# Optimization experiments

Hardware: AMD Instinct MI355X
Metric: run time of the kernel (lower is better)

## Reference

```python
import jax, jax.numpy as jnp
import numpy as np
from jax import lax

WINDOW = 8
MAX_VAL = 1.0
C1 = (0.01 * MAX_VAL) ** 2
C2 = (0.03 * MAX_VAL) ** 2


def _box_sum(x):
    # Equivalent to conv2d with an all-ones WINDOW x WINDOW kernel, groups=C, VALID padding.
    return lax.reduce_window(x, 0.0, lax.add,
                             window_dimensions=(1, 1, WINDOW, WINDOW),
                             window_strides=(1, 1, 1, 1),
                             padding='VALID')


def setup_inputs() -> dict:
    key = jax.random.key(0)
    k1, k2 = jax.random.split(key)
    shape = (32, 3, 512, 512)  # NCHW, C=3 per groups=3 conv
    groundtruth = jax.random.uniform(k1, shape, dtype=jnp.float32)
    noisy_img = jax.random.uniform(k2, shape, dtype=jnp.float32)
    return {"groundtruth": groundtruth, "noisy_img": noisy_img}


def reference(groundtruth, noisy_img):
    mu1 = _box_sum(groundtruth)
    mu2 = _box_sum(noisy_img)
    mu1_sq = mu1 * mu1
    mu2_sq = mu2 * mu2
    mu1_mu2 = mu1 * mu2
    sigma1_sq = _box_sum(groundtruth * groundtruth) - mu1_sq
    sigma2_sq = _box_sum(noisy_img * noisy_img) - mu2_sq
    sigma12 = _box_sum(groundtruth * noisy_img) - mu1_mu2
    ssim_map = ((2.0 * mu1_mu2 + C1) * (2.0 * sigma12 + C2)) / (
        (mu1_sq + mu2_sq + C1) * (sigma1_sq + sigma2_sq + C2))
    return jnp.mean(1.0 - ssim_map)
```

## Files before the change

### kernel.cpp

```cpp
#include <hip/hip_runtime.h>


#define W 512
#define H 512
#define OW 505
#define OH 505
#define TH 16
#define NSTRIP ((OH + TH - 1) / TH)
#define NIMG 96
#define NPIX (96.0 * 505.0 * 505.0)

__device__ __forceinline__ float4 ld4(const float* p) { return *(const float4*)p; }
__device__ __forceinline__ float4 f4add(float4 a, float4 b) {
    return make_float4(a.x + b.x, a.y + b.y, a.z + b.z, a.w + b.w);
}
__device__ __forceinline__ float4 f4sub(float4 a, float4 b) {
    return make_float4(a.x - b.x, a.y - b.y, a.z - b.z, a.w - b.w);
}
__device__ __forceinline__ float4 f4mul(float4 a, float4 b) {
    return make_float4(a.x * b.x, a.y * b.y, a.z * b.z, a.w * b.w);
}

__global__ void finalize(const double* p, float* out) {
    out[0] = 1.0f - (float)(*p / NPIX);
}

__global__ void __launch_bounds__(128, 2)
ssim_main(const float* __restrict__ gt, const float* __restrict__ ni,
          double* __restrict__ acc_out)
{
    const int t   = threadIdx.x;
    const int c0  = t * 4;
    const int img = blockIdx.y;
    const int R0  = blockIdx.x * TH;
    const int R1  = min(R0 + TH, OH);

    const float C1 = 1e-4f;
    const float C2 = 9e-4f;

    const float* gx = gt + (size_t)img * (W * H) + c0;
    const float* gy = ni + (size_t)img * (W * H) + c0;

    __shared__ float vbuf[4][4][520];
    __shared__ float wpart[2];

    float4 ring_x[8], ring_y[8];
    float4 vsx = make_float4(0, 0, 0, 0);
    float4 vsy = make_float4(0, 0, 0, 0);
    float4 vsq = make_float4(0, 0, 0, 0);
    float4 vsp = make_float4(0, 0, 0, 0);

#pragma unroll
    for (int k = 0; k < 7; ++k) {
        float4 x = ld4(gx + (size_t)(R0 + k) * W);
        float4 y = ld4(gy + (size_t)(R0 + k) * W);
        ring_x[k] = x; ring_y[k] = y;
        vsx = f4add(vsx, x);
        vsy = f4add(vsy, y);
        vsq = f4add(vsq, f4add(f4mul(x, x), f4mul(y, y)));
        vsp = f4add(vsp, f4mul(x, y));
    }
    ring_x[7] = make_float4(0, 0, 0, 0);
    ring_y[7] = make_float4(0, 0, 0, 0);

    float4 pfx[4], pfy[4];
#pragma unroll
    for (int m = 0; m < 4; ++m) {
        pfx[m] = ld4(gx + (size_t)(R0 + 7 + m) * W);
        pfy[m] = ld4(gy + (size_t)(R0 + 7 + m) * W);
    }

    float acc = 0.0f;

#define PHASEA_ROW(rb, m, slot) {                                         \
        if ((rb) + (m) < R1) {                         \
            float4 cx = pfx[m], cy = pfy[m];                              \
            float4 ox = ring_x[slot], oy = ring_y[slot];                  \
            vsx = f4add(f4sub(vsx, ox), cx);                              \
            vsy = f4add(f4sub(vsy, oy), cy);                              \
            vsq = f4add(vsq, f4sub(f4add(f4mul(cx, cx), f4mul(cy, cy)),   \
                                   f4add(f4mul(ox, ox), f4mul(oy, oy)))); \
            vsp = f4add(vsp, f4sub(f4mul(cx, cy), f4mul(ox, oy)));        \
            ring_x[slot] = cx; ring_y[slot] = cy;                         \
            *(float4*)&vbuf[m][0][c0] = vsx;                              \
            *(float4*)&vbuf[m][1][c0] = vsy;                              \
            *(float4*)&vbuf[m][2][c0] = vsq;                              \
            *(float4*)&vbuf[m][3][c0] = vsp;                              \
        }                                                                 \
    }

#define HORIZ(q) {                                                        \
        float4 o = *(float4*)&vbuf[m][q][c0];                             \
        float4 a = *(float4*)&vbuf[m][q][c0 + 4];                         \
        float4 e = *(float4*)&vbuf[m][q][c0 + 8];                         \
        float s = ((o.x + o.y) + (o.z + o.w)) +                           \
                  ((a.x + a.y) + (a.z + a.w));                            \
        B[q][0] = s;                                                      \
        s += e.x - o.x; B[q][1] = s;                                      \
        s += e.y - o.y; B[q][2] = s;                                      \
        s += e.z - o.z; B[q][3] = s;                                      \
    }

#define PHASEB_ROW(rb, mm) {                                              \
        if ((rb) + (mm) < R1) {                        \
            const int m = (mm);                                           \
            float B[4][4];                                                \
            HORIZ(0) HORIZ(1) HORIZ(2) HORIZ(3)                           \
            _Pragma("unroll")                                             \
            for (int j = 0; j < 4; ++j) {                                 \
                float Sx = B[0][j], Sy = B[1][j];                         \
                float Sq = B[2][j], Sp = B[3][j];                         \
                float mu12 = Sx * Sy;                                     \
                float n1v = 2.0f * mu12 + C1;                             \
                float n2v = 2.0f * (Sp - mu12) + C2;                      \
                float sx2 = Sx * Sx, sy2 = Sy * Sy;                       \
                float d1  = sx2 + sy2 + C1;                               \
                float d2  = (Sq - sx2 - sy2) + C2;                        \
                float sv  = (n1v * n2v) * __builtin_amdgcn_rcpf(d1 * d2); \
                if (c0 + j < OW) acc += sv;                               \
            }                                                             \
        }                                                                 \
    }

#define GROUP(rb, s0, s1, s2, s3) {                                       \
        if ((rb) < R1) {                               \
            PHASEA_ROW(rb, 0, s0) PHASEA_ROW(rb, 1, s1)                   \
            PHASEA_ROW(rb, 2, s2) PHASEA_ROW(rb, 3, s3)                   \
            __syncthreads();                                              \
            _Pragma("unroll")                                             \
            for (int m = 0; m < 4; ++m) {      \
                if ((rb) + 4 + m < R1) {                                  \
                    pfx[m] = ld4(gx + (size_t)((rb) + 11 + m) * W);       \
                    pfy[m] = ld4(gy + (size_t)((rb) + 11 + m) * W);       \
                }                                                         \
            }                                                             \
            PHASEB_ROW(rb, 0) PHASEB_ROW(rb, 1)                           \
            PHASEB_ROW(rb, 2) PHASEB_ROW(rb, 3)                           \
            __syncthreads();                                              \
        }                                                                 \
    }

    for (int rb0 = R0; rb0 < R1; rb0 += 8) {
        GROUP(rb0,     7, 0, 1, 2)
        GROUP(rb0 + 4, 3, 4, 5, 6)
    }

#pragma unroll
    for (int off = 32; off > 0; off >>= 1) acc += __shfl_down(acc, off);
    const int wave = t >> 6, lane = t & 63;
    if (lane == 0) wpart[wave] = acc;
    __syncthreads();
    if (t == 0) atomicAdd(acc_out, (double)(wpart[0] + wpart[1]));
}

extern "C" void kernel_launch(void* const* d_in, const int* in_sizes, int n_in,
                              void* d_out, int out_size, void* d_ws, size_t ws_size,
                              hipStream_t stream) {
    const float* gt = (const float*)d_in[0];
    const float* ni = (const float*)d_in[1];
    double* acc = (double*)d_ws;

    hipMemsetAsync(acc, 0, sizeof(double), stream);
    dim3 grid(NSTRIP, NIMG);
    ssim_main<<<grid, 128, 0, stream>>>(gt, ni, acc);
    finalize<<<1, 1, 0, stream>>>(acc, (float*)d_out);
}
```

Before: 232.8 us.

## Process two rows per group with lighter barriers and higher occupancy

Each group now handles two output rows instead of four, which halves the shared vertical-sum buffer and the prefetch registers. Launch bounds are raised to allow four blocks per CU. __syncthreads is replaced by a barrier that waits only on LDS counters, so outstanding global prefetch loads are not drained at each barrier. The cost is twice as many barriers per row, and prefetch now runs only two rows ahead, which shortens the latency-hiding window.

```diff
diff --git a/kernel.cpp b/kernel.cpp
--- a/kernel.cpp
+++ b/kernel.cpp
@@ -21,11 +21,16 @@
     return make_float4(a.x * b.x, a.y * b.y, a.z * b.z, a.w * b.w);
 }
 
+__device__ __forceinline__ void wbar() {
+    asm volatile("s_waitcnt lgkmcnt(0)" ::: "memory");
+    __builtin_amdgcn_s_barrier();
+}
+
 __global__ void finalize(const double* p, float* out) {
     out[0] = 1.0f - (float)(*p / NPIX);
 }
 
-__global__ void __launch_bounds__(128, 2)
+__global__ void __launch_bounds__(128, 4)
 ssim_main(const float* __restrict__ gt, const float* __restrict__ ni,
           double* __restrict__ acc_out)
 {
@@ -41,7 +46,7 @@
     const float* gx = gt + (size_t)img * (W * H) + c0;
     const float* gy = ni + (size_t)img * (W * H) + c0;
 
-    __shared__ float vbuf[4][4][520];
+    __shared__ float vbuf[2][4][520];
     __shared__ float wpart[2];
 
     float4 ring_x[8], ring_y[8];
@@ -63,12 +68,11 @@
     ring_x[7] = make_float4(0, 0, 0, 0);
     ring_y[7] = make_float4(0, 0, 0, 0);
 
-    float4 pfx[4], pfy[4];
-#pragma unroll
-    for (int m = 0; m < 4; ++m) {
-        pfx[m] = ld4(gx + (size_t)(R0 + 7 + m) * W);
-        pfy[m] = ld4(gy + (size_t)(R0 + 7 + m) * W);
-    }
+    float4 pfx[2], pfy[2];
+    pfx[0] = ld4(gx + (size_t)(R0 + 7) * W);
+    pfy[0] = ld4(gy + (size_t)(R0 + 7) * W);
+    pfx[1] = ld4(gx + (size_t)(R0 + 8) * W);
+    pfy[1] = ld4(gy + (size_t)(R0 + 8) * W);
 
     float acc = 0.0f;
 
@@ -122,27 +126,28 @@
         }                                                                 \
     }
 
-#define GROUP(rb, s0, s1, s2, s3) {                                       \
+#define GROUP2(rb, s0, s1) {                                              \
         if ((rb) < R1) {                               \
             PHASEA_ROW(rb, 0, s0) PHASEA_ROW(rb, 1, s1)                   \
-            PHASEA_ROW(rb, 2, s2) PHASEA_ROW(rb, 3, s3)                   \
-            __syncthreads();                                              \
-            _Pragma("unroll")                                             \
-            for (int m = 0; m < 4; ++m) {      \
-                if ((rb) + 4 + m < R1) {                                  \
-                    pfx[m] = ld4(gx + (size_t)((rb) + 11 + m) * W);       \
-                    pfy[m] = ld4(gy + (size_t)((rb) + 11 + m) * W);       \
-                }                                                         \
+            wbar();                                                       \
+            if ((rb) + 2 < R1) {                                          \
+                pfx[0] = ld4(gx + (size_t)((rb) + 9) * W);                \
+                pfy[0] = ld4(gy + (size_t)((rb) + 9) * W);                \
+            }                                                             \
+            if ((rb) + 3 < R1) {                                          \
+                pfx[1] = ld4(gx + (size_t)((rb) + 10) * W);               \
+                pfy[1] = ld4(gy + (size_t)((rb) + 10) * W);               \
             }                                                             \
             PHASEB_ROW(rb, 0) PHASEB_ROW(rb, 1)                           \
-            PHASEB_ROW(rb, 2) PHASEB_ROW(rb, 3)                           \
-            __syncthreads();                                              \
+            wbar();                                                       \
         }                                                                 \
     }
 
     for (int rb0 = R0; rb0 < R1; rb0 += 8) {
-        GROUP(rb0,     7, 0, 1, 2)
-        GROUP(rb0 + 4, 3, 4, 5, 6)
+        GROUP2(rb0,     7, 0)
+        GROUP2(rb0 + 2, 1, 2)
+        GROUP2(rb0 + 4, 3, 4)
+        GROUP2(rb0 + 6, 5, 6)
     }
 
 #pragma unroll
```

After: 251.1 us. 1.08x slower.

## Replace shared-memory horizontal sums with wave shuffles, single-wave blocks

Applied to the files above, without the earlier changes.

Each block becomes a single 64-lane wave where every lane owns 8 columns, so a row of 512 fits in one wave. The horizontal window sum now reads the neighbour lane's vertical sums through shuffles instead of shared memory, which removes the LDS buffer and both __syncthreads per row group. The ring buffer of old rows is dropped: the row leaving the window is reloaded from global memory (expected to hit cache). Costs are twice the loads per row and higher register pressure from holding 8 columns of 4 sums per lane.

```diff
diff --git a/kernel.cpp b/kernel.cpp
--- a/kernel.cpp
+++ b/kernel.cpp
@@ -11,26 +11,22 @@
 #define NPIX (96.0 * 505.0 * 505.0)
 
 __device__ __forceinline__ float4 ld4(const float* p) { return *(const float4*)p; }
-__device__ __forceinline__ float4 f4add(float4 a, float4 b) {
-    return make_float4(a.x + b.x, a.y + b.y, a.z + b.z, a.w + b.w);
-}
-__device__ __forceinline__ float4 f4sub(float4 a, float4 b) {
-    return make_float4(a.x - b.x, a.y - b.y, a.z - b.z, a.w - b.w);
-}
-__device__ __forceinline__ float4 f4mul(float4 a, float4 b) {
-    return make_float4(a.x * b.x, a.y * b.y, a.z * b.z, a.w * b.w);
-}
 
 __global__ void finalize(const double* p, float* out) {
     out[0] = 1.0f - (float)(*p / NPIX);
 }
 
-__global__ void __launch_bounds__(128, 2)
+#define UNPACK8(a0, a1, dst) {                                            \
+        dst[0] = a0.x; dst[1] = a0.y; dst[2] = a0.z; dst[3] = a0.w;       \
+        dst[4] = a1.x; dst[5] = a1.y; dst[6] = a1.z; dst[7] = a1.w;       \
+    }
+
+__global__ void __launch_bounds__(64, 4)
 ssim_main(const float* __restrict__ gt, const float* __restrict__ ni,
           double* __restrict__ acc_out)
 {
-    const int t   = threadIdx.x;
-    const int c0  = t * 4;
+    const int l   = threadIdx.x;
+    const int c0  = l * 8;
     const int img = blockIdx.y;
     const int R0  = blockIdx.x * TH;
     const int R1  = min(R0 + TH, OH);
@@ -41,116 +37,133 @@
     const float* gx = gt + (size_t)img * (W * H) + c0;
     const float* gy = ni + (size_t)img * (W * H) + c0;
 
-    __shared__ float vbuf[4][4][520];
-    __shared__ float wpart[2];
+    float vsx[8], vsy[8], vsq[8], vsp[8];
+#pragma unroll
+    for (int j = 0; j < 8; ++j) { vsx[j] = 0.f; vsy[j] = 0.f; vsq[j] = 0.f; vsp[j] = 0.f; }
 
-    float4 ring_x[8], ring_y[8];
-    float4 vsx = make_float4(0, 0, 0, 0);
-    float4 vsy = make_float4(0, 0, 0, 0);
-    float4 vsq = make_float4(0, 0, 0, 0);
-    float4 vsp = make_float4(0, 0, 0, 0);
+    float4 pix0, pix1, piy0, piy1;
+    float4 pox0, pox1, poy0, poy1;
 
-#pragma unroll
-    for (int k = 0; k < 7; ++k) {
-        float4 x = ld4(gx + (size_t)(R0 + k) * W);
-        float4 y = ld4(gy + (size_t)(R0 + k) * W);
-        ring_x[k] = x; ring_y[k] = y;
-        vsx = f4add(vsx, x);
-        vsy = f4add(vsy, y);
-        vsq = f4add(vsq, f4add(f4mul(x, x), f4mul(y, y)));
-        vsp = f4add(vsp, f4mul(x, y));
-    }
-    ring_x[7] = make_float4(0, 0, 0, 0);
-    ring_y[7] = make_float4(0, 0, 0, 0);
-
-    float4 pfx[4], pfy[4];
-#pragma unroll
-    for (int m = 0; m < 4; ++m) {
-        pfx[m] = ld4(gx + (size_t)(R0 + 7 + m) * W);
-        pfy[m] = ld4(gy + (size_t)(R0 + 7 + m) * W);
+    {
+        const float* px = gx + (size_t)R0 * W;
+        const float* py = gy + (size_t)R0 * W;
+        pix0 = ld4(px); pix1 = ld4(px + 4);
+        piy0 = ld4(py); piy1 = ld4(py + 4);
     }
 
     float acc = 0.0f;
 
-#define PHASEA_ROW(rb, m, slot) {                                         \
-        if ((rb) + (m) < R1) {                         \
-            float4 cx = pfx[m], cy = pfy[m];                              \
-            float4 ox = ring_x[slot], oy = ring_y[slot];                  \
-            vsx = f4add(f4sub(vsx, ox), cx);                              \
-            vsy = f4add(f4sub(vsy, oy), cy);                              \
-            vsq = f4add(vsq, f4sub(f4add(f4mul(cx, cx), f4mul(cy, cy)),   \
-                                   f4add(f4mul(ox, ox), f4mul(oy, oy)))); \
-            vsp = f4add(vsp, f4sub(f4mul(cx, cy), f4mul(ox, oy)));        \
-            ring_x[slot] = cx; ring_y[slot] = cy;                         \
-            *(float4*)&vbuf[m][0][c0] = vsx;                              \
-            *(float4*)&vbuf[m][1][c0] = vsy;                              \
-            *(float4*)&vbuf[m][2][c0] = vsq;                              \
-            *(float4*)&vbuf[m][3][c0] = vsp;                              \
+#pragma unroll 1
+    for (int r = R0; r < R0 + 7; ++r) {
+        float cx[8], cy[8];
+        UNPACK8(pix0, pix1, cx)
+        UNPACK8(piy0, piy1, cy)
+        {
+            const float* px = gx + (size_t)(r + 1) * W;
+            const float* py = gy + (size_t)(r + 1) * W;
+            pix0 = ld4(px); pix1 = ld4(px + 4);
+            piy0 = ld4(py); piy1 = ld4(py + 4);
+        }
+#pragma unroll
+        for (int j = 0; j < 8; ++j) {
+            vsx[j] = vsx[j] + cx[j];
+            vsy[j] = vsy[j] + cy[j];
+            vsq[j] = vsq[j] + (cx[j] * cx[j] + cy[j] * cy[j]);
+            vsp[j] = vsp[j] + cx[j] * cy[j];
+        }
+    }
+
+#define HORIZ_SSIM() {                                                    \
+        float nx[8], ny[8], nq[8], np_[8];                                \
+        _Pragma("unroll")                                                 \
+        for (int j = 0; j < 8; ++j) {                                     \
+            nx[j]  = __shfl_down(vsx[j], 1);                              \
+            ny[j]  = __shfl_down(vsy[j], 1);                              \
+            nq[j]  = __shfl_down(vsq[j], 1);                              \
+            np_[j] = __shfl_down(vsp[j], 1);                              \
+        }                                                                 \
+        float Sx = ((vsx[0] + vsx[1]) + (vsx[2] + vsx[3])) +              \
+                   ((vsx[4] + vsx[5]) + (vsx[6] + vsx[7]));               \
+        float Sy = ((vsy[0] + vsy[1]) + (vsy[2] + vsy[3])) +              \
+                   ((vsy[4] + vsy[5]) + (vsy[6] + vsy[7]));               \
+        float Sq = ((vsq[0] + vsq[1]) + (vsq[2] + vsq[3])) +              \
+                   ((vsq[4] + vsq[5]) + (vsq[6] + vsq[7]));               \
+        float Sp = ((vsp[0] + vsp[1]) + (vsp[2] + vsp[3])) +              \
+                   ((vsp[4] + vsp[5]) + (vsp[6] + vsp[7]));               \
+        _Pragma("unroll")                                                 \
+        for (int j = 0; j < 8; ++j) {                                     \
+            if (j) {                                                      \
+                Sx += nx[j-1] - vsx[j-1];                                 \
+                Sy += ny[j-1] - vsy[j-1];                                 \
+                Sq += nq[j-1] - vsq[j-1];                                 \
+                Sp += np_[j-1] - vsp[j-1];                                \
+            }                                                             \
+            float mu12 = Sx * Sy;                                         \
+            float n1v = 2.0f * mu12 + C1;                                 \
+            float n2v = 2.0f * (Sp - mu12) + C2;                          \
+            float sx2 = Sx * Sx, sy2 = Sy * Sy;                           \
+            float d1  = sx2 + sy2 + C1;                                   \
+            float d2  = (Sq - sx2 - sy2) + C2;                            \
+            float sv  = (n1v * n2v) * __builtin_amdgcn_rcpf(d1 * d2);     \
+            if (c0 + j < OW) acc += sv;                                   \
         }                                                                 \
     }
 
-#define HORIZ(q) {                                                        \
-        float4 o = *(float4*)&vbuf[m][q][c0];                             \
-        float4 a = *(float4*)&vbuf[m][q][c0 + 4];                         \
-        float4 e = *(float4*)&vbuf[m][q][c0 + 8];                         \
-        float s = ((o.x + o.y) + (o.z + o.w)) +                           \
-                  ((a.x + a.y) + (a.z + a.w));                            \
-        B[q][0] = s;                                                      \
-        s += e.x - o.x; B[q][1] = s;                                      \
-        s += e.y - o.y; B[q][2] = s;                                      \
-        s += e.z - o.z; B[q][3] = s;                                      \
+    {
+        float cx[8], cy[8];
+        UNPACK8(pix0, pix1, cx)
+        UNPACK8(piy0, piy1, cy)
+        {
+            const float* px = gx + (size_t)(R0 + 8) * W;
+            const float* py = gy + (size_t)(R0 + 8) * W;
+            pix0 = ld4(px); pix1 = ld4(px + 4);
+            piy0 = ld4(py); piy1 = ld4(py + 4);
+            const float* qx = gx + (size_t)R0 * W;
+            const float* qy = gy + (size_t)R0 * W;
+            pox0 = ld4(qx); pox1 = ld4(qx + 4);
+            poy0 = ld4(qy); poy1 = ld4(qy + 4);
+        }
+#pragma unroll
+        for (int j = 0; j < 8; ++j) {
+            vsx[j] = vsx[j] + cx[j];
+            vsy[j] = vsy[j] + cy[j];
+            vsq[j] = vsq[j] + (cx[j] * cx[j] + cy[j] * cy[j]);
+            vsp[j] = vsp[j] + cx[j] * cy[j];
+        }
+        HORIZ_SSIM()
     }
 
-#define PHASEB_ROW(rb, mm) {                                              \
-        if ((rb) + (mm) < R1) {                        \
-            const int m = (mm);                                           \
-            float B[4][4];                                                \
-            HORIZ(0) HORIZ(1) HORIZ(2) HORIZ(3)                           \
-            _Pragma("unroll")                                             \
-            for (int j = 0; j < 4; ++j) {                                 \
-                float Sx = B[0][j], Sy = B[1][j];                         \
-                float Sq = B[2][j], Sp = B[3][j];                         \
-                float mu12 = Sx * Sy;                                     \
-                float n1v = 2.0f * mu12 + C1;                             \
-                float n2v = 2.0f * (Sp - mu12) + C2;                      \
-                float sx2 = Sx * Sx, sy2 = Sy * Sy;                       \
-                float d1  = sx2 + sy2 + C1;                               \
-                float d2  = (Sq - sx2 - sy2) + C2;                        \
-                float sv  = (n1v * n2v) * __builtin_amdgcn_rcpf(d1 * d2); \
-                if (c0 + j < OW) acc += sv;                               \
-            }                                                             \
-        }                                                                 \
-    }
-
-#define GROUP(rb, s0, s1, s2, s3) {                                       \
-        if ((rb) < R1) {                               \
-            PHASEA_ROW(rb, 0, s0) PHASEA_ROW(rb, 1, s1)                   \
-            PHASEA_ROW(rb, 2, s2) PHASEA_ROW(rb, 3, s3)                   \
-            __syncthreads();                                              \
-            _Pragma("unroll")                                             \
-            for (int m = 0; m < 4; ++m) {      \
-                if ((rb) + 4 + m < R1) {                                  \
-                    pfx[m] = ld4(gx + (size_t)((rb) + 11 + m) * W);       \
-                    pfy[m] = ld4(gy + (size_t)((rb) + 11 + m) * W);       \
-                }                                                         \
-            }                                                             \
-            PHASEB_ROW(rb, 0) PHASEB_ROW(rb, 1)                           \
-            PHASEB_ROW(rb, 2) PHASEB_ROW(rb, 3)                           \
-            __syncthreads();                                              \
-        }                                                                 \
-    }
-
-    for (int rb0 = R0; rb0 < R1; rb0 += 8) {
-        GROUP(rb0,     7, 0, 1, 2)
-        GROUP(rb0 + 4, 3, 4, 5, 6)
+#pragma unroll 1
+    for (int o = R0 + 1; o < R1; ++o) {
+        float cx[8], cy[8], ox[8], oy[8];
+        UNPACK8(pix0, pix1, cx)
+        UNPACK8(piy0, piy1, cy)
+        UNPACK8(pox0, pox1, ox)
+        UNPACK8(poy0, poy1, oy)
+        if (o + 1 < R1) {
+            const float* px = gx + (size_t)(o + 8) * W;
+            const float* py = gy + (size_t)(o + 8) * W;
+            pix0 = ld4(px); pix1 = ld4(px + 4);
+            piy0 = ld4(py); piy1 = ld4(py + 4);
+            const float* qx = gx + (size_t)o * W;
+            const float* qy = gy + (size_t)o * W;
+            pox0 = ld4(qx); pox1 = ld4(qx + 4);
+            poy0 = ld4(qy); poy1 = ld4(qy + 4);
+        }
+#pragma unroll
+        for (int j = 0; j < 8; ++j) {
+            vsx[j] = (vsx[j] - ox[j]) + cx[j];
+            vsy[j] = (vsy[j] - oy[j]) + cy[j];
+            vsq[j] = vsq[j] + ((cx[j] * cx[j] + cy[j] * cy[j]) -
+                               (ox[j] * ox[j] + oy[j] * oy[j]));
+            vsp[j] = vsp[j] + (cx[j] * cy[j] - ox[j] * oy[j]);
+        }
+        HORIZ_SSIM()
     }
 
 #pragma unroll
     for (int off = 32; off > 0; off >>= 1) acc += __shfl_down(acc, off);
-    const int wave = t >> 6, lane = t & 63;
-    if (lane == 0) wpart[wave] = acc;
-    __syncthreads();
-    if (t == 0) atomicAdd(acc_out, (double)(wpart[0] + wpart[1]));
+    if (l == 0) atomicAdd(acc_out, (double)acc);
 }
 
 extern "C" void kernel_launch(void* const* d_in, const int* in_sizes, int n_in,
@@ -162,6 +175,6 @@
 
     hipMemsetAsync(acc, 0, sizeof(double), stream);
     dim3 grid(NSTRIP, NIMG);
-    ssim_main<<<grid, 128, 0, stream>>>(gt, ni, acc);
+    ssim_main<<<grid, 64, 0, stream>>>(gt, ni, acc);
     finalize<<<1, 1, 0, stream>>>(acc, (float*)d_out);
 }
```

Result: slower. 319.0 us (+37.0%).

## Use single-wave column slabs with shuffle-based horizontal box sums

Applied to the files above, without the earlier changes.

Replaces the 128-thread, 4-columns-per-thread strip kernel, which staged vertical sums in shared memory behind barriers, with 64-thread single-wave workgroups. Each workgroup covers a 64-column slab with a 7-column halo (57 outputs) and a quarter of the rows. Horizontal 8-wide sums are built with three shuffle-down steps, so there is no LDS traffic and no __syncthreads. Loads become scalar per lane, about 12% of the columns are reloaded as halo, and block IDs are remapped with an interleaved swizzle. The main risks are more redundant loads and more blocks doing atomics.

```diff
diff --git a/kernel.cpp b/kernel.cpp
--- a/kernel.cpp
+++ b/kernel.cpp
@@ -5,152 +5,120 @@
 #define H 512
 #define OW 505
 #define OH 505
-#define TH 16
-#define NSTRIP ((OH + TH - 1) / TH)
 #define NIMG 96
+#define NSLAB 9
+#define NSPLIT 4
+#define NWG (NSLAB * NSPLIT * NIMG)
 #define NPIX (96.0 * 505.0 * 505.0)
-
-__device__ __forceinline__ float4 ld4(const float* p) { return *(const float4*)p; }
-__device__ __forceinline__ float4 f4add(float4 a, float4 b) {
-    return make_float4(a.x + b.x, a.y + b.y, a.z + b.z, a.w + b.w);
-}
-__device__ __forceinline__ float4 f4sub(float4 a, float4 b) {
-    return make_float4(a.x - b.x, a.y - b.y, a.z - b.z, a.w - b.w);
-}
-__device__ __forceinline__ float4 f4mul(float4 a, float4 b) {
-    return make_float4(a.x * b.x, a.y * b.y, a.z * b.z, a.w * b.w);
-}
 
 __global__ void finalize(const double* p, float* out) {
     out[0] = 1.0f - (float)(*p / NPIX);
 }
 
-__global__ void __launch_bounds__(128, 2)
+__global__ void __launch_bounds__(64)
 ssim_main(const float* __restrict__ gt, const float* __restrict__ ni,
           double* __restrict__ acc_out)
 {
-    const int t   = threadIdx.x;
-    const int c0  = t * 4;
-    const int img = blockIdx.y;
-    const int R0  = blockIdx.x * TH;
-    const int R1  = min(R0 + TH, OH);
+    const int l = threadIdx.x;
+
+    const int b     = blockIdx.x;
+    const int wid   = (b & 7) * (NWG / 8) + (b >> 3);
+    const int img   = wid / (NSLAB * NSPLIT);
+    const int rem   = wid % (NSLAB * NSPLIT);
+    const int slab  = rem % NSLAB;
+    const int split = rem / NSLAB;
+
+    const int x0   = slab * 57;
+    const int col  = x0 + l;
+    const int cole = min(col, W - 1);
+    const int cmax = min(x0 + 57, OW);
+    const bool valid = col < cmax;
+
+    const int r0 = split * 127;
+    const int R1 = min(r0 + 127, OH);
 
     const float C1 = 1e-4f;
     const float C2 = 9e-4f;
 
-    const float* gx = gt + (size_t)img * (W * H) + c0;
-    const float* gy = ni + (size_t)img * (W * H) + c0;
+    const float* gx = gt + (size_t)img * (W * H) + cole;
+    const float* gy = ni + (size_t)img * (W * H) + cole;
 
-    __shared__ float vbuf[4][4][520];
-    __shared__ float wpart[2];
+    float rgx[8], rgy[8];
+    float vsx = 0.f, vsy = 0.f, vsq = 0.f, vsp = 0.f;
 
-    float4 ring_x[8], ring_y[8];
-    float4 vsx = make_float4(0, 0, 0, 0);
-    float4 vsy = make_float4(0, 0, 0, 0);
-    float4 vsq = make_float4(0, 0, 0, 0);
-    float4 vsp = make_float4(0, 0, 0, 0);
+    float pfx[4], pfy[4];
 
+    float wx[7], wy[7];
 #pragma unroll
     for (int k = 0; k < 7; ++k) {
-        float4 x = ld4(gx + (size_t)(R0 + k) * W);
-        float4 y = ld4(gy + (size_t)(R0 + k) * W);
-        ring_x[k] = x; ring_y[k] = y;
-        vsx = f4add(vsx, x);
-        vsy = f4add(vsy, y);
-        vsq = f4add(vsq, f4add(f4mul(x, x), f4mul(y, y)));
-        vsp = f4add(vsp, f4mul(x, y));
+        wx[k] = gx[(size_t)(r0 + k) * W];
+        wy[k] = gy[(size_t)(r0 + k) * W];
     }
-    ring_x[7] = make_float4(0, 0, 0, 0);
-    ring_y[7] = make_float4(0, 0, 0, 0);
-
-    float4 pfx[4], pfy[4];
 #pragma unroll
-    for (int m = 0; m < 4; ++m) {
-        pfx[m] = ld4(gx + (size_t)(R0 + 7 + m) * W);
-        pfy[m] = ld4(gy + (size_t)(R0 + 7 + m) * W);
+    for (int s = 0; s < 4; ++s) {
+        pfx[s] = gx[(size_t)(r0 + 7 + s) * W];
+        pfy[s] = gy[(size_t)(r0 + 7 + s) * W];
     }
+#pragma unroll
+    for (int k = 0; k < 7; ++k) {
+        float cx = wx[k], cy = wy[k];
+        rgx[k] = cx; rgy[k] = cy;
+        vsx += cx; vsy += cy;
+        vsq += cx * cx + cy * cy;
+        vsp += cx * cy;
+    }
+    rgx[7] = 0.f; rgy[7] = 0.f;
 
     float acc = 0.0f;
 
-#define PHASEA_ROW(rb, m, slot) {                                         \
-        if ((rb) + (m) < R1) {                         \
-            float4 cx = pfx[m], cy = pfy[m];                              \
-            float4 ox = ring_x[slot], oy = ring_y[slot];                  \
-            vsx = f4add(f4sub(vsx, ox), cx);                              \
-            vsy = f4add(f4sub(vsy, oy), cy);                              \
-            vsq = f4add(vsq, f4sub(f4add(f4mul(cx, cx), f4mul(cy, cy)),   \
-                                   f4add(f4mul(ox, ox), f4mul(oy, oy)))); \
-            vsp = f4add(vsp, f4sub(f4mul(cx, cy), f4mul(ox, oy)));        \
-            ring_x[slot] = cx; ring_y[slot] = cy;                         \
-            *(float4*)&vbuf[m][0][c0] = vsx;                              \
-            *(float4*)&vbuf[m][1][c0] = vsy;                              \
-            *(float4*)&vbuf[m][2][c0] = vsq;                              \
-            *(float4*)&vbuf[m][3][c0] = vsp;                              \
+#define PREFIX_SSIM() {                                                   \
+        float s1x = vsx + __shfl_down(vsx, 1);                            \
+        float s1y = vsy + __shfl_down(vsy, 1);                            \
+        float s1q = vsq + __shfl_down(vsq, 1);                            \
+        float s1p = vsp + __shfl_down(vsp, 1);                            \
+        float s2x = s1x + __shfl_down(s1x, 2);                            \
+        float s2y = s1y + __shfl_down(s1y, 2);                            \
+        float s2q = s1q + __shfl_down(s1q, 2);                            \
+        float s2p = s1p + __shfl_down(s1p, 2);                            \
+        float Sx  = s2x + __shfl_down(s2x, 4);                            \
+        float Sy  = s2y + __shfl_down(s2y, 4);                            \
+        float Sq  = s2q + __shfl_down(s2q, 4);                            \
+        float Sp  = s2p + __shfl_down(s2p, 4);                            \
+        float mu12 = Sx * Sy;                                             \
+        float n1v = 2.0f * mu12 + C1;                                     \
+        float n2v = 2.0f * (Sp - mu12) + C2;                              \
+        float sx2 = Sx * Sx, sy2 = Sy * Sy;                               \
+        float d1  = sx2 + sy2 + C1;                                       \
+        float d2  = (Sq - sx2 - sy2) + C2;                                \
+        float sv  = (n1v * n2v) * __builtin_amdgcn_rcpf(d1 * d2);         \
+        if (valid) acc += sv;                                             \
+    }
+
+#define ROW(k) {                                                          \
+        const int o = rb + (k);                                           \
+        if (o < R1) {                                   \
+            float cx = pfx[(k) & 3], cy = pfy[(k) & 3];                   \
+            float ox = rgx[((k) + 7) & 7], oy = rgy[((k) + 7) & 7];       \
+            vsx = (vsx - ox) + cx;                                        \
+            vsy = (vsy - oy) + cy;                                        \
+            vsq = vsq + ((cx * cx + cy * cy) - (ox * ox + oy * oy));      \
+            vsp = vsp + (cx * cy - ox * oy);                              \
+            rgx[((k) + 7) & 7] = cx; rgy[((k) + 7) & 7] = cy;             \
+            if (o + 4 < R1) {                                             \
+                pfx[(k) & 3] = gx[(size_t)(o + 11) * W];                  \
+                pfy[(k) & 3] = gy[(size_t)(o + 11) * W];                  \
+            }                                                             \
+            PREFIX_SSIM()                                                 \
         }                                                                 \
     }
 
-#define HORIZ(q) {                                                        \
-        float4 o = *(float4*)&vbuf[m][q][c0];                             \
-        float4 a = *(float4*)&vbuf[m][q][c0 + 4];                         \
-        float4 e = *(float4*)&vbuf[m][q][c0 + 8];                         \
-        float s = ((o.x + o.y) + (o.z + o.w)) +                           \
-                  ((a.x + a.y) + (a.z + a.w));                            \
-        B[q][0] = s;                                                      \
-        s += e.x - o.x; B[q][1] = s;                                      \
-        s += e.y - o.y; B[q][2] = s;                                      \
-        s += e.z - o.z; B[q][3] = s;                                      \
-    }
-
-#define PHASEB_ROW(rb, mm) {                                              \
-        if ((rb) + (mm) < R1) {                        \
-            const int m = (mm);                                           \
-            float B[4][4];                                                \
-            HORIZ(0) HORIZ(1) HORIZ(2) HORIZ(3)                           \
-            _Pragma("unroll")                                             \
-            for (int j = 0; j < 4; ++j) {                                 \
-                float Sx = B[0][j], Sy = B[1][j];                         \
-                float Sq = B[2][j], Sp = B[3][j];                         \
-                float mu12 = Sx * Sy;                                     \
-                float n1v = 2.0f * mu12 + C1;                             \
-                float n2v = 2.0f * (Sp - mu12) + C2;                      \
-                float sx2 = Sx * Sx, sy2 = Sy * Sy;                       \
-                float d1  = sx2 + sy2 + C1;                               \
-                float d2  = (Sq - sx2 - sy2) + C2;                        \
-                float sv  = (n1v * n2v) * __builtin_amdgcn_rcpf(d1 * d2); \
-                if (c0 + j < OW) acc += sv;                               \
-            }                                                             \
-        }                                                                 \
-    }
-
-#define GROUP(rb, s0, s1, s2, s3) {                                       \
-        if ((rb) < R1) {                               \
-            PHASEA_ROW(rb, 0, s0) PHASEA_ROW(rb, 1, s1)                   \
-            PHASEA_ROW(rb, 2, s2) PHASEA_ROW(rb, 3, s3)                   \
-            __syncthreads();                                              \
-            _Pragma("unroll")                                             \
-            for (int m = 0; m < 4; ++m) {      \
-                if ((rb) + 4 + m < R1) {                                  \
-                    pfx[m] = ld4(gx + (size_t)((rb) + 11 + m) * W);       \
-                    pfy[m] = ld4(gy + (size_t)((rb) + 11 + m) * W);       \
-                }                                                         \
-            }                                                             \
-            PHASEB_ROW(rb, 0) PHASEB_ROW(rb, 1)                           \
-            PHASEB_ROW(rb, 2) PHASEB_ROW(rb, 3)                           \
-            __syncthreads();                                              \
-        }                                                                 \
-    }
-
-    for (int rb0 = R0; rb0 < R1; rb0 += 8) {
-        GROUP(rb0,     7, 0, 1, 2)
-        GROUP(rb0 + 4, 3, 4, 5, 6)
+    for (int rb = r0; rb < R1; rb += 8) {
+        ROW(0) ROW(1) ROW(2) ROW(3) ROW(4) ROW(5) ROW(6) ROW(7)
     }
 
 #pragma unroll
     for (int off = 32; off > 0; off >>= 1) acc += __shfl_down(acc, off);
-    const int wave = t >> 6, lane = t & 63;
-    if (lane == 0) wpart[wave] = acc;
-    __syncthreads();
-    if (t == 0) atomicAdd(acc_out, (double)(wpart[0] + wpart[1]));
+    if (l == 0) atomicAdd(acc_out, (double)acc);
 }
 
 extern "C" void kernel_launch(void* const* d_in, const int* in_sizes, int n_in,
@@ -161,7 +129,6 @@
     double* acc = (double*)d_ws;
 
     hipMemsetAsync(acc, 0, sizeof(double), stream);
-    dim3 grid(NSTRIP, NIMG);
-    ssim_main<<<grid, 128, 0, stream>>>(gt, ni, acc);
+    ssim_main<<<dim3(NWG), 64, 0, stream>>>(gt, ni, acc);
     finalize<<<1, 1, 0, stream>>>(acc, (float*)d_out);
 }
```

Measured after the change: 301.1 us. +29.3%, slower.
